# Performance work log

Hardware: AMD Instinct MI355X
Metric: run time of the kernel (lower is better)

Reference implementation:

```python
import jax, jax.numpy as jnp
import numpy as np

Q_HEADS, KV_HEADS, HEAD_SIZE, H, MAX_LEN = 16, 4, 64, 1024, 4096
B, S = 1, 4096


def _rope_tables(max_len, head_size):
    half = head_size // 2
    inv_freq = 1.0 / (10000.0 ** (np.arange(half, dtype=np.float32) / half))
    pos = np.arange(max_len, dtype=np.float32)
    ang = pos[:, None] * inv_freq[None, :]  # [max_len, half]
    return jnp.asarray(np.sin(ang)), jnp.asarray(np.cos(ang))


def setup_inputs() -> dict:
    key = jax.random.key(0)
    ks = jax.random.split(key, 6)
    sc = 1.0 / np.sqrt(H)
    x = jax.random.normal(ks[0], (B, S, H), dtype=jnp.float32)
    wq = jax.random.normal(ks[1], (H, H), dtype=jnp.float32) * sc
    wk = jax.random.normal(ks[2], (H, KV_HEADS * HEAD_SIZE), dtype=jnp.float32) * sc
    wv = jax.random.normal(ks[3], (H, KV_HEADS * HEAD_SIZE), dtype=jnp.float32) * sc
    wo = jax.random.normal(ks[4], (H, H), dtype=jnp.float32) * sc
    sin, cos = _rope_tables(MAX_LEN, HEAD_SIZE)
    full_mask = jnp.tril(jnp.ones((MAX_LEN, MAX_LEN), dtype=bool))
    attention_mask = jnp.ones((B, S), dtype=jnp.int32)
    return {"x": x, "attention_mask": attention_mask, "start": 0,
            "wq": wq, "wk": wk, "wv": wv, "wo": wo,
            "sin": sin, "cos": cos, "full_mask": full_mask}


def _rotate(t, sin, cos, start):
    # t: [b, heads, s, head_size]; interleaved even/odd RoPE
    s = t.shape[2]
    sn = sin[start:start + s, :][None, None, :, :]
    cs = cos[start:start + s, :][None, None, :, :]
    even, odd = t[..., 0::2], t[..., 1::2]
    out_even = cs * even - sn * odd
    out_odd = sn * even + cs * odd
    return jnp.stack((out_even, out_odd), axis=-1).reshape(t.shape)


def _expand_kv(t, group):
    # [b, kv_heads, s, d] -> [b, kv_heads*group, s, d]
    b, kvh, s, d = t.shape
    return jnp.broadcast_to(t[:, :, None], (b, kvh, group, s, d)).reshape(b, kvh * group, s, d)


def reference(x, attention_mask, start, wq, wk, wv, wo, sin, cos, full_mask):
    b, s, _ = x.shape
    group = Q_HEADS // KV_HEADS
    Q = (x @ wq).reshape(b, s, Q_HEADS, HEAD_SIZE).transpose(0, 2, 1, 3)
    K = (x @ wk).reshape(b, s, KV_HEADS, HEAD_SIZE).transpose(0, 2, 1, 3)
    V = (x @ wv).reshape(b, s, KV_HEADS, HEAD_SIZE).transpose(0, 2, 1, 3)
    Q = _rotate(Q, sin, cos, start)
    K = _rotate(K, sin, cos, start)
    K = _expand_kv(K, group)
    V = _expand_kv(V, group)
    z = jnp.einsum('bhqd,bhkd->bhqk', Q, K) / (HEAD_SIZE ** 0.5)
    kv_len = start + s
    mask = full_mask[:s, :kv_len][None, None, :, :]
    amask = (attention_mask[:, :kv_len] != 0)[:, None, None, :]
    mask = mask & amask
    z = jnp.where(mask, z, -1000000.0)
    A = jax.nn.softmax(z, axis=-1)
    ctx = jnp.einsum('bhqk,bhkd->bhqd', A, V)
    q_mask = attention_mask[:, :s].astype(ctx.dtype)[:, None, :, None]
    ctx = ctx * q_mask
    ctx = ctx.transpose(0, 2, 1, 3).reshape(b, s, H)
    return ctx @ wo
```

## Files before the change

kernel.cpp:

```cpp
#include <hip/hip_runtime.h>

typedef __bf16 bf16x8 __attribute__((ext_vector_type(8)));
typedef float f32x4 __attribute__((ext_vector_type(4)));
typedef unsigned int u32x4 __attribute__((ext_vector_type(4)));

typedef const void __attribute__((address_space(1)))* gas1;
typedef void __attribute__((address_space(3)))* las3;

__device__ __forceinline__ unsigned short f2bf(float f) {
  unsigned int u = __builtin_bit_cast(unsigned int, f);
  u += 0x7fffu + ((u >> 16) & 1u);
  return (unsigned short)(u >> 16);
}
__device__ __forceinline__ float bf2f(unsigned short h) {
  unsigned int u = ((unsigned int)h) << 16;
  return __builtin_bit_cast(float, u);
}
__device__ __forceinline__ unsigned int pack2bf(float lo, float hi) {
  return (unsigned int)f2bf(lo) | ((unsigned int)f2bf(hi) << 16);
}
__device__ __forceinline__ unsigned int packtr(float lo, float hi) {
  return __builtin_amdgcn_perm(__builtin_bit_cast(unsigned int, hi),
                               __builtin_bit_cast(unsigned int, lo), 0x07060302u);
}

__global__ __launch_bounds__(256) void prep(const float* __restrict__ x,
                                            const float* __restrict__ wq,
                                            const float* __restrict__ wk,
                                            const float* __restrict__ wv,
                                            const float* __restrict__ wo,
                                            unsigned short* __restrict__ xb,
                                            unsigned short* __restrict__ wtqkv,
                                            unsigned short* __restrict__ wot) {
  __shared__ float tile[32][33];
  const int b = blockIdx.x;
  const int tid = threadIdx.x;
  if (b < 4096) {
    int i = b * 256 + tid;
    float4 v = ((const float4*)x)[i];
    uint2 o;
    o.x = pack2bf(v.x, v.y);
    o.y = pack2bf(v.z, v.w);
    ((uint2*)xb)[i] = o;
    return;
  }
  const float* src;
  unsigned short* dst;
  int R, C, t;
  if (b < 5120)      { t = b - 4096; src = wq; dst = wtqkv;               R = 1024; C = 1024; }
  else if (b < 5376) { t = b - 5120; src = wk; dst = wtqkv + 1024 * 1024; R = 1024; C = 256; }
  else if (b < 5632) { t = b - 5376; src = wv; dst = wtqkv + 1280 * 1024; R = 1024; C = 256; }
  else               { t = b - 5632; src = wo; dst = wot;                 R = 1024; C = 1024; }
  const int ntc = C >> 5;
  const int c0 = (t % ntc) * 32, r0 = (t / ntc) * 32;
  const int tx = tid & 31, ty = tid >> 5;
#pragma unroll
  for (int i = 0; i < 4; ++i)
    tile[ty + i * 8][tx] = src[(r0 + ty + i * 8) * C + c0 + tx];
  __syncthreads();
#pragma unroll
  for (int i = 0; i < 4; ++i)
    dst[(c0 + ty + i * 8) * R + r0 + tx] = f2bf(tile[tx][ty + i * 8]);
}

__global__ __launch_bounds__(256, 2) void gemm_bt2(const unsigned short* __restrict__ A,
                                                   const unsigned short* __restrict__ Bt,
                                                   void* __restrict__ Cout,
                                                   int M, int N, int K, int outF32) {
  __shared__ __align__(16) unsigned short Als[128 * 32];
  __shared__ __align__(16) unsigned short Bls[128 * 32];
  const int tid = threadIdx.x;
  const int wave = tid >> 6, lane = tid & 63;
  const int lgrp = lane >> 4, lmod = lane & 15;
  const int wm = (wave & 1) * 64, wn = (wave >> 1) * 64;
  const int m0 = blockIdx.y * 128, n0 = blockIdx.x * 128;

  f32x4 acc[4][4] = {};

  for (int k0 = 0; k0 < K; k0 += 32) {
    __syncthreads();
#pragma unroll
    for (int it = 0; it < 2; ++it) {
      int idx = tid + it * 256;
      int rr = idx >> 2, cc = (idx & 3) * 8;
      __builtin_amdgcn_global_load_lds((gas1)(const void*)&A[(size_t)(m0 + rr) * K + k0 + cc],
                                       (las3)(void*)&Als[(it * 256 + wave * 64) * 8], 16, 0, 0);
      __builtin_amdgcn_global_load_lds((gas1)(const void*)&Bt[(size_t)(n0 + rr) * K + k0 + cc],
                                       (las3)(void*)&Bls[(it * 256 + wave * 64) * 8], 16, 0, 0);
    }
    __syncthreads();
    bf16x8 af[4], bfr[4];
#pragma unroll
    for (int mi = 0; mi < 4; ++mi)
      af[mi] = __builtin_bit_cast(bf16x8, *(const u32x4*)&Als[(wm + mi * 16 + lmod) * 32 + lgrp * 8]);
#pragma unroll
    for (int ni = 0; ni < 4; ++ni)
      bfr[ni] = __builtin_bit_cast(bf16x8, *(const u32x4*)&Bls[(wn + ni * 16 + lmod) * 32 + lgrp * 8]);
#pragma unroll
    for (int mi = 0; mi < 4; ++mi)
#pragma unroll
      for (int ni = 0; ni < 4; ++ni)
        acc[mi][ni] = __builtin_amdgcn_mfma_f32_16x16x32_bf16(af[mi], bfr[ni], acc[mi][ni], 0, 0, 0);
  }

#pragma unroll
  for (int mi = 0; mi < 4; ++mi)
#pragma unroll
    for (int ni = 0; ni < 4; ++ni)
#pragma unroll
      for (int r = 0; r < 4; ++r) {
        int row = m0 + wm + mi * 16 + lgrp * 4 + r;
        int col = n0 + wn + ni * 16 + lmod;
        float v = acc[mi][ni][r];
        if (outF32) ((float*)Cout)[(size_t)row * N + col] = v;
        else ((unsigned short*)Cout)[(size_t)row * N + col] = f2bf(v);
      }
}

__global__ __launch_bounds__(256) void rope_vt(const unsigned short* __restrict__ qkv,
                                               const float* __restrict__ sinT,
                                               const float* __restrict__ cosT,
                                               unsigned short* __restrict__ Qh,
                                               unsigned short* __restrict__ Kh,
                                               unsigned short* __restrict__ Vt) {
  __shared__ unsigned short tile[32][33];
  const int b = blockIdx.x;
  const int tid = threadIdx.x;
  if (b < 5120) {
    const float qscale = 0.18033688011112042f;
    int u = b * 256 + tid;
    int s = u / 320, cu = u % 320;
    int col = cu * 4;
    uint2 pr = *(const uint2*)&qkv[s * 1536 + col];
    float e0 = bf2f((unsigned short)(pr.x & 0xffff));
    float o0 = bf2f((unsigned short)(pr.x >> 16));
    float e1 = bf2f((unsigned short)(pr.y & 0xffff));
    float o1 = bf2f((unsigned short)(pr.y >> 16));
    if (col < 1024) {
      int h = col >> 6, d = col & 63, i0 = d >> 1;
      float sn0 = sinT[s * 32 + i0], cs0 = cosT[s * 32 + i0];
      float sn1 = sinT[s * 32 + i0 + 1], cs1 = cosT[s * 32 + i0 + 1];
      uint2 w;
      w.x = pack2bf((cs0 * e0 - sn0 * o0) * qscale, (sn0 * e0 + cs0 * o0) * qscale);
      w.y = pack2bf((cs1 * e1 - sn1 * o1) * qscale, (sn1 * e1 + cs1 * o1) * qscale);
      *(uint2*)&Qh[(h * 4096 + s) * 64 + d] = w;
    } else {
      int c = col - 1024;
      int h = c >> 6, d = c & 63, i0 = d >> 1;
      float sn0 = sinT[s * 32 + i0], cs0 = cosT[s * 32 + i0];
      float sn1 = sinT[s * 32 + i0 + 1], cs1 = cosT[s * 32 + i0 + 1];
      uint2 w;
      w.x = pack2bf(cs0 * e0 - sn0 * o0, sn0 * e0 + cs0 * o0);
      w.y = pack2bf(cs1 * e1 - sn1 * o1, sn1 * e1 + cs1 * o1);
      *(uint2*)&Kh[(h * 4096 + s) * 64 + d] = w;
    }
    return;
  }
  int t = b - 5120;
  int h = t >> 8, rem = t & 255;
  int d0 = (rem >> 7) * 32, s0 = (rem & 127) * 32;
  int tx = tid & 31, ty = tid >> 5;
#pragma unroll
  for (int i = 0; i < 4; ++i)
    tile[ty + i * 8][tx] = qkv[(s0 + ty + i * 8) * 1536 + 1280 + h * 64 + d0 + tx];
  __syncthreads();
#pragma unroll
  for (int i = 0; i < 4; ++i)
    Vt[(h * 64 + d0 + ty + i * 8) * 4096 + s0 + tx] = tile[tx][ty + i * 8];
}

__global__ __launch_bounds__(256, 2) void attn3(const unsigned short* __restrict__ Qh,
                                                const unsigned short* __restrict__ Kh,
                                                const unsigned short* __restrict__ Vt,
                                                unsigned short* __restrict__ ctx) {
  __shared__ __align__(16) unsigned short Kls[128 * 68];
  __shared__ __align__(16) unsigned short Vls[64 * 136];
  const int bx = blockIdx.x;
  const int head = bx & 15;
  const int qidx = bx >> 4;
  const int qb = (qidx < 16) ? (31 - qidx) : (qidx - 16);
  const int kvh = head >> 2;
  const int tid = threadIdx.x;
  const int wave = tid >> 6, lane = tid & 63;
  const int lgrp = lane >> 4, lmod = lane & 15;
  const int qbase = qb * 128;

  const unsigned short* Kg = Kh + (size_t)kvh * 4096 * 64;
  const unsigned short* Vg = Vt + (size_t)kvh * 64 * 4096;

  bf16x8 qf[2][2];
  int qrow[2];
#pragma unroll
  for (int qt = 0; qt < 2; ++qt) {
    qrow[qt] = qbase + wave * 32 + qt * 16 + lmod;
    const unsigned short* Qg = Qh + ((size_t)head * 4096 + qrow[qt]) * 64;
    qf[qt][0] = __builtin_bit_cast(bf16x8, *(const u32x4*)&Qg[lgrp * 8]);
    qf[qt][1] = __builtin_bit_cast(bf16x8, *(const u32x4*)&Qg[32 + lgrp * 8]);
  }

  const int kbase = (8 * (lmod >> 2) + (lmod & 3)) * 68 + lgrp * 8;
  const int vbase = lmod * 136 + lgrp * 8;

  f32x4 accO[2][4] = {};
  float m_i[2] = {-3e38f, -3e38f}, l_i[2] = {0.f, 0.f};

  for (int kc = 0; kc <= qb; ++kc) {
    const int kb = kc * 128;
    __syncthreads();
#pragma unroll
    for (int i = 0; i < 4; ++i) {
      int ii = tid + i * 256;
      int r = ii >> 3, sg = (ii & 7) * 8;
      u32x4 dK = *(const u32x4*)&Kg[(size_t)(kb + r) * 64 + sg];
      uint2* pd = (uint2*)&Kls[r * 68 + sg];
      pd[0] = make_uint2(dK[0], dK[1]);
      pd[1] = make_uint2(dK[2], dK[3]);
    }
#pragma unroll
    for (int i = 0; i < 4; ++i) {
      int ii = tid + i * 256;
      int r = ii >> 4, sg = (ii & 15) * 8;
      *(u32x4*)&Vls[r * 136 + sg] = *(const u32x4*)&Vg[(size_t)r * 4096 + kb + sg];
    }
    __syncthreads();

    f32x4 s[4][2][2];
#pragma unroll
    for (int g = 0; g < 4; ++g)
#pragma unroll
      for (int t = 0; t < 2; ++t) {
        const unsigned short* ka = &Kls[kbase + (32 * g + 4 * t) * 68];
        uint2 a0 = *(const uint2*)&ka[0];
        uint2 a1 = *(const uint2*)&ka[4];
        uint2 b0 = *(const uint2*)&ka[32];
        uint2 b1 = *(const uint2*)&ka[36];
        u32x4 lo = {a0.x, a0.y, a1.x, a1.y};
        u32x4 hi = {b0.x, b0.y, b1.x, b1.y};
        bf16x8 alo = __builtin_bit_cast(bf16x8, lo);
        bf16x8 ahi = __builtin_bit_cast(bf16x8, hi);
#pragma unroll
        for (int qt = 0; qt < 2; ++qt) {
          f32x4 z = {};
          z = __builtin_amdgcn_mfma_f32_16x16x32_bf16(alo, qf[qt][0], z, 0, 0, 0);
          z = __builtin_amdgcn_mfma_f32_16x16x32_bf16(ahi, qf[qt][1], z, 0, 0, 0);
          s[g][t][qt] = z;
        }
      }

#pragma unroll
    for (int qt = 0; qt < 2; ++qt) {
      if (kb + 127 > qbase + wave * 32 + qt * 16) {
#pragma unroll
        for (int g = 0; g < 4; ++g)
#pragma unroll
          for (int t = 0; t < 2; ++t)
#pragma unroll
            for (int r = 0; r < 4; ++r) {
              int key = kb + 32 * g + 8 * lgrp + 4 * t + r;
              if (key > qrow[qt]) s[g][t][qt][r] = -3e38f;
            }
      }
    }

#pragma unroll
    for (int qt = 0; qt < 2; ++qt) {
      f32x4 v0 = s[0][0][qt], v1 = s[0][1][qt];
#pragma unroll
      for (int g = 1; g < 4; ++g)
#pragma unroll
        for (int r = 0; r < 4; ++r) {
          v0[r] = fmaxf(v0[r], s[g][0][qt][r]);
          v1[r] = fmaxf(v1[r], s[g][1][qt][r]);
        }
      float mx = fmaxf(fmaxf(fmaxf(v0[0], v0[1]), fmaxf(v0[2], v0[3])),
                       fmaxf(fmaxf(v1[0], v1[1]), fmaxf(v1[2], v1[3])));
      mx = fmaxf(mx, __shfl_xor(mx, 16, 64));
      mx = fmaxf(mx, __shfl_xor(mx, 32, 64));
      float mnew = fmaxf(m_i[qt], mx);
      float alpha = __builtin_amdgcn_exp2f(m_i[qt] - mnew);
      m_i[qt] = mnew;
      f32x4 su = {};
#pragma unroll
      for (int g = 0; g < 4; ++g)
#pragma unroll
        for (int t = 0; t < 2; ++t)
#pragma unroll
          for (int r = 0; r < 4; ++r) {
            float ev = __builtin_amdgcn_exp2f(s[g][t][qt][r] - mnew);
            s[g][t][qt][r] = ev;
            su[r] += ev;
          }
      float rs = (su[0] + su[1]) + (su[2] + su[3]);
      rs += __shfl_xor(rs, 16, 64);
      rs += __shfl_xor(rs, 32, 64);
      l_i[qt] = l_i[qt] * alpha + rs;
#pragma unroll
      for (int dt = 0; dt < 4; ++dt)
#pragma unroll
        for (int r = 0; r < 4; ++r) accO[qt][dt][r] *= alpha;
    }

#pragma unroll
    for (int g = 0; g < 4; ++g) {
      bf16x8 pf[2];
#pragma unroll
      for (int qt = 0; qt < 2; ++qt) {
        u32x4 pk;
        pk[0] = packtr(s[g][0][qt][0], s[g][0][qt][1]);
        pk[1] = packtr(s[g][0][qt][2], s[g][0][qt][3]);
        pk[2] = packtr(s[g][1][qt][0], s[g][1][qt][1]);
        pk[3] = packtr(s[g][1][qt][2], s[g][1][qt][3]);
        pf[qt] = __builtin_bit_cast(bf16x8, pk);
      }
#pragma unroll
      for (int dt = 0; dt < 4; ++dt) {
        bf16x8 vf = __builtin_bit_cast(bf16x8, *(const u32x4*)&Vls[vbase + dt * 2176 + 32 * g]);
        accO[0][dt] = __builtin_amdgcn_mfma_f32_16x16x32_bf16(vf, pf[0], accO[0][dt], 0, 0, 0);
        accO[1][dt] = __builtin_amdgcn_mfma_f32_16x16x32_bf16(vf, pf[1], accO[1][dt], 0, 0, 0);
      }
    }
  }

#pragma unroll
  for (int qt = 0; qt < 2; ++qt) {
    float inv = 1.f / l_i[qt];
#pragma unroll
    for (int dt = 0; dt < 4; ++dt) {
      uint2 o;
      o.x = pack2bf(accO[qt][dt][0] * inv, accO[qt][dt][1] * inv);
      o.y = pack2bf(accO[qt][dt][2] * inv, accO[qt][dt][3] * inv);
      *(uint2*)&ctx[(size_t)qrow[qt] * 1024 + head * 64 + dt * 16 + lgrp * 4] = o;
    }
  }
}

extern "C" void kernel_launch(void* const* d_in, const int* in_sizes, int n_in,
                              void* d_out, int out_size, void* d_ws, size_t ws_size,
                              hipStream_t stream) {
  const float* x    = (const float*)d_in[0];
  const float* wq   = (const float*)d_in[3];
  const float* wk   = (const float*)d_in[4];
  const float* wv   = (const float*)d_in[5];
  const float* wo   = (const float*)d_in[6];
  const float* sinT = (const float*)d_in[7];
  const float* cosT = (const float*)d_in[8];

  unsigned short* ws    = (unsigned short*)d_ws;
  unsigned short* xb    = ws;
  unsigned short* wtqkv = xb + 4096 * 1024;
  unsigned short* wot   = wtqkv + 1536 * 1024;
  unsigned short* qkv   = wot + 1024 * 1024;
  unsigned short* Qh    = qkv + 4096 * 1536;
  unsigned short* Kh    = Qh + 16 * 4096 * 64;
  unsigned short* Vt    = Kh + 4 * 4096 * 64;
  unsigned short* ctx   = Vt + 4 * 64 * 4096;
  float* out = (float*)d_out;

  prep<<<6656, 256, 0, stream>>>(x, wq, wk, wv, wo, xb, wtqkv, wot);
  gemm_bt2<<<dim3(12, 32), 256, 0, stream>>>(xb, wtqkv, qkv, 4096, 1536, 1024, 0);
  rope_vt<<<6144, 256, 0, stream>>>(qkv, sinT, cosT, Qh, Kh, Vt);
  attn3<<<dim3(512), 256, 0, stream>>>(Qh, Kh, Vt, ctx);
  gemm_bt2<<<dim3(8, 32), 256, 0, stream>>>(ctx, wot, out, 4096, 1024, 1024, 1);
}
```

Baseline: 258.1 us.

## Fuse RoPE and V transpose into QKV GEMM epilogue; retile GEMMs and attention

The QKV projection GEMM now writes rotated, scaled Q and K and transposed V directly, which removes the separate rope_vt kernel and the intermediate qkv buffer round trip. sin and cos are interleaved into one float2 table during prep. Both GEMMs move to 128x64 tiles with more blocks and higher occupancy bounds. Attention switches to 128-thread blocks covering 64 query rows each, with a new causal ordering of query blocks for load balance. The epilogue stores are scattered 2-byte writes and use shuffles, and the smaller tiles reduce data reuse per block.

```diff
diff --git a/kernel.cpp b/kernel.cpp
--- a/kernel.cpp
+++ b/kernel.cpp
@@ -29,9 +29,12 @@
                                             const float* __restrict__ wk,
                                             const float* __restrict__ wv,
                                             const float* __restrict__ wo,
+                                            const float* __restrict__ sinT,
+                                            const float* __restrict__ cosT,
                                             unsigned short* __restrict__ xb,
                                             unsigned short* __restrict__ wtqkv,
-                                            unsigned short* __restrict__ wot) {
+                                            unsigned short* __restrict__ wot,
+                                            float2* __restrict__ scT) {
   __shared__ float tile[32][33];
   const int b = blockIdx.x;
   const int tid = threadIdx.x;
@@ -44,6 +47,11 @@
     ((uint2*)xb)[i] = o;
     return;
   }
+  if (b >= 6656) {
+    int idx = (b - 6656) * 256 + tid;
+    scT[idx] = make_float2(sinT[idx], cosT[idx]);
+    return;
+  }
   const float* src;
   unsigned short* dst;
   int R, C, t;
@@ -63,113 +71,144 @@
     dst[(c0 + ty + i * 8) * R + r0 + tx] = f2bf(tile[tx][ty + i * 8]);
 }
 
-__global__ __launch_bounds__(256, 2) void gemm_bt2(const unsigned short* __restrict__ A,
+__global__ __launch_bounds__(256, 3) void gemm_qkv(const unsigned short* __restrict__ A,
                                                    const unsigned short* __restrict__ Bt,
-                                                   void* __restrict__ Cout,
-                                                   int M, int N, int K, int outF32) {
+                                                   const float2* __restrict__ scT,
+                                                   unsigned short* __restrict__ Qh,
+                                                   unsigned short* __restrict__ Kh,
+                                                   unsigned short* __restrict__ Vt) {
   __shared__ __align__(16) unsigned short Als[128 * 32];
-  __shared__ __align__(16) unsigned short Bls[128 * 32];
+  __shared__ __align__(16) unsigned short Bls[64 * 32];
+  const int K = 1024;
   const int tid = threadIdx.x;
   const int wave = tid >> 6, lane = tid & 63;
   const int lgrp = lane >> 4, lmod = lane & 15;
-  const int wm = (wave & 1) * 64, wn = (wave >> 1) * 64;
-  const int m0 = blockIdx.y * 128, n0 = blockIdx.x * 128;
-
-  f32x4 acc[4][4] = {};
+  const int wm = (wave & 1) * 64, wn = (wave >> 1) * 32;
+  const int m0 = blockIdx.y * 128, n0 = blockIdx.x * 64;
+  const int rr = tid >> 2, cc = (tid & 3) * 8;
+
+  f32x4 acc[4][2] = {};
 
   for (int k0 = 0; k0 < K; k0 += 32) {
     __syncthreads();
 #pragma unroll
     for (int it = 0; it < 2; ++it) {
       int idx = tid + it * 256;
-      int rr = idx >> 2, cc = (idx & 3) * 8;
-      __builtin_amdgcn_global_load_lds((gas1)(const void*)&A[(size_t)(m0 + rr) * K + k0 + cc],
+      __builtin_amdgcn_global_load_lds((gas1)(const void*)&A[(size_t)(m0 + (idx >> 2)) * K + k0 + cc],
                                        (las3)(void*)&Als[(it * 256 + wave * 64) * 8], 16, 0, 0);
-      __builtin_amdgcn_global_load_lds((gas1)(const void*)&Bt[(size_t)(n0 + rr) * K + k0 + cc],
-                                       (las3)(void*)&Bls[(it * 256 + wave * 64) * 8], 16, 0, 0);
-    }
-    __syncthreads();
-    bf16x8 af[4], bfr[4];
+    }
+    __builtin_amdgcn_global_load_lds((gas1)(const void*)&Bt[(size_t)(n0 + rr) * K + k0 + cc],
+                                     (las3)(void*)&Bls[(wave * 64) * 8], 16, 0, 0);
+    __syncthreads();
+    bf16x8 af[4], bfr[2];
 #pragma unroll
     for (int mi = 0; mi < 4; ++mi)
       af[mi] = __builtin_bit_cast(bf16x8, *(const u32x4*)&Als[(wm + mi * 16 + lmod) * 32 + lgrp * 8]);
 #pragma unroll
-    for (int ni = 0; ni < 4; ++ni)
+    for (int ni = 0; ni < 2; ++ni)
       bfr[ni] = __builtin_bit_cast(bf16x8, *(const u32x4*)&Bls[(wn + ni * 16 + lmod) * 32 + lgrp * 8]);
 #pragma unroll
     for (int mi = 0; mi < 4; ++mi)
 #pragma unroll
-      for (int ni = 0; ni < 4; ++ni)
+      for (int ni = 0; ni < 2; ++ni)
         acc[mi][ni] = __builtin_amdgcn_mfma_f32_16x16x32_bf16(af[mi], bfr[ni], acc[mi][ni], 0, 0, 0);
   }
 
+  const int cbase = n0;
+  if (cbase >= 1280) {
+    const int kvh = (cbase - 1280) >> 6;
+#pragma unroll
+    for (int mi = 0; mi < 4; ++mi)
+#pragma unroll
+      for (int ni = 0; ni < 2; ++ni) {
+        int d = wn + ni * 16 + lmod;
+        int s = m0 + wm + mi * 16 + lgrp * 4;
+        uint2 o;
+        o.x = pack2bf(acc[mi][ni][0], acc[mi][ni][1]);
+        o.y = pack2bf(acc[mi][ni][2], acc[mi][ni][3]);
+        *(uint2*)&Vt[((size_t)(kvh * 64 + d)) * 4096 + s] = o;
+      }
+    return;
+  }
+
+  const float qscale = 0.18033688011112042f;
+  const bool isQ = (cbase < 1024);
+  const int h = isQ ? (cbase >> 6) : ((cbase - 1024) >> 6);
+  unsigned short* dstbase = isQ ? Qh : Kh;
+  const bool evn = (lmod & 1) == 0;
 #pragma unroll
   for (int mi = 0; mi < 4; ++mi)
 #pragma unroll
-    for (int ni = 0; ni < 4; ++ni)
+    for (int ni = 0; ni < 2; ++ni) {
+      int d = ((cbase & 63) + wn + ni * 16 + lmod) & 63;
+      int i = d >> 1;
+#pragma unroll
+      for (int r = 0; r < 4; ++r) {
+        float v = acc[mi][ni][r];
+        float pp = __shfl_xor(v, 1, 64);
+        int rl = wm + mi * 16 + lgrp * 4 + r;
+        float2 sc = scT[(size_t)(m0 + rl) * 32 + i];
+        float e = evn ? v : pp, o = evn ? pp : v;
+        float outv = evn ? (sc.y * e - sc.x * o) : (sc.x * e + sc.y * o);
+        if (isQ) outv *= qscale;
+        dstbase[((size_t)h * 4096 + m0 + rl) * 64 + d] = f2bf(outv);
+      }
+    }
+}
+
+__global__ __launch_bounds__(256, 3) void gemm_out(const unsigned short* __restrict__ A,
+                                                   const unsigned short* __restrict__ Bt,
+                                                   float* __restrict__ Cout) {
+  __shared__ __align__(16) unsigned short Als[128 * 32];
+  __shared__ __align__(16) unsigned short Bls[64 * 32];
+  const int K = 1024, N = 1024;
+  const int tid = threadIdx.x;
+  const int wave = tid >> 6, lane = tid & 63;
+  const int lgrp = lane >> 4, lmod = lane & 15;
+  const int wm = (wave & 1) * 64, wn = (wave >> 1) * 32;
+  const int m0 = blockIdx.y * 128, n0 = blockIdx.x * 64;
+  const int rr = tid >> 2, cc = (tid & 3) * 8;
+
+  f32x4 acc[4][2] = {};
+
+  for (int k0 = 0; k0 < K; k0 += 32) {
+    __syncthreads();
+#pragma unroll
+    for (int it = 0; it < 2; ++it) {
+      int idx = tid + it * 256;
+      __builtin_amdgcn_global_load_lds((gas1)(const void*)&A[(size_t)(m0 + (idx >> 2)) * K + k0 + cc],
+                                       (las3)(void*)&Als[(it * 256 + wave * 64) * 8], 16, 0, 0);
+    }
+    __builtin_amdgcn_global_load_lds((gas1)(const void*)&Bt[(size_t)(n0 + rr) * K + k0 + cc],
+                                     (las3)(void*)&Bls[(wave * 64) * 8], 16, 0, 0);
+    __syncthreads();
+    bf16x8 af[4], bfr[2];
+#pragma unroll
+    for (int mi = 0; mi < 4; ++mi)
+      af[mi] = __builtin_bit_cast(bf16x8, *(const u32x4*)&Als[(wm + mi * 16 + lmod) * 32 + lgrp * 8]);
+#pragma unroll
+    for (int ni = 0; ni < 2; ++ni)
+      bfr[ni] = __builtin_bit_cast(bf16x8, *(const u32x4*)&Bls[(wn + ni * 16 + lmod) * 32 + lgrp * 8]);
+#pragma unroll
+    for (int mi = 0; mi < 4; ++mi)
+#pragma unroll
+      for (int ni = 0; ni < 2; ++ni)
+        acc[mi][ni] = __builtin_amdgcn_mfma_f32_16x16x32_bf16(af[mi], bfr[ni], acc[mi][ni], 0, 0, 0);
+  }
+
+#pragma unroll
+  for (int mi = 0; mi < 4; ++mi)
+#pragma unroll
+    for (int ni = 0; ni < 2; ++ni)
 #pragma unroll
       for (int r = 0; r < 4; ++r) {
         int row = m0 + wm + mi * 16 + lgrp * 4 + r;
         int col = n0 + wn + ni * 16 + lmod;
-        float v = acc[mi][ni][r];
-        if (outF32) ((float*)Cout)[(size_t)row * N + col] = v;
-        else ((unsigned short*)Cout)[(size_t)row * N + col] = f2bf(v);
-      }
-}
-
-__global__ __launch_bounds__(256) void rope_vt(const unsigned short* __restrict__ qkv,
-                                               const float* __restrict__ sinT,
-                                               const float* __restrict__ cosT,
-                                               unsigned short* __restrict__ Qh,
-                                               unsigned short* __restrict__ Kh,
-                                               unsigned short* __restrict__ Vt) {
-  __shared__ unsigned short tile[32][33];
-  const int b = blockIdx.x;
-  const int tid = threadIdx.x;
-  if (b < 5120) {
-    const float qscale = 0.18033688011112042f;
-    int u = b * 256 + tid;
-    int s = u / 320, cu = u % 320;
-    int col = cu * 4;
-    uint2 pr = *(const uint2*)&qkv[s * 1536 + col];
-    float e0 = bf2f((unsigned short)(pr.x & 0xffff));
-    float o0 = bf2f((unsigned short)(pr.x >> 16));
-    float e1 = bf2f((unsigned short)(pr.y & 0xffff));
-    float o1 = bf2f((unsigned short)(pr.y >> 16));
-    if (col < 1024) {
-      int h = col >> 6, d = col & 63, i0 = d >> 1;
-      float sn0 = sinT[s * 32 + i0], cs0 = cosT[s * 32 + i0];
-      float sn1 = sinT[s * 32 + i0 + 1], cs1 = cosT[s * 32 + i0 + 1];
-      uint2 w;
-      w.x = pack2bf((cs0 * e0 - sn0 * o0) * qscale, (sn0 * e0 + cs0 * o0) * qscale);
-      w.y = pack2bf((cs1 * e1 - sn1 * o1) * qscale, (sn1 * e1 + cs1 * o1) * qscale);
-      *(uint2*)&Qh[(h * 4096 + s) * 64 + d] = w;
-    } else {
-      int c = col - 1024;
-      int h = c >> 6, d = c & 63, i0 = d >> 1;
-      float sn0 = sinT[s * 32 + i0], cs0 = cosT[s * 32 + i0];
-      float sn1 = sinT[s * 32 + i0 + 1], cs1 = cosT[s * 32 + i0 + 1];
-      uint2 w;
-      w.x = pack2bf(cs0 * e0 - sn0 * o0, sn0 * e0 + cs0 * o0);
-      w.y = pack2bf(cs1 * e1 - sn1 * o1, sn1 * e1 + cs1 * o1);
-      *(uint2*)&Kh[(h * 4096 + s) * 64 + d] = w;
-    }
-    return;
-  }
-  int t = b - 5120;
-  int h = t >> 8, rem = t & 255;
-  int d0 = (rem >> 7) * 32, s0 = (rem & 127) * 32;
-  int tx = tid & 31, ty = tid >> 5;
-#pragma unroll
-  for (int i = 0; i < 4; ++i)
-    tile[ty + i * 8][tx] = qkv[(s0 + ty + i * 8) * 1536 + 1280 + h * 64 + d0 + tx];
-  __syncthreads();
-#pragma unroll
-  for (int i = 0; i < 4; ++i)
-    Vt[(h * 64 + d0 + ty + i * 8) * 4096 + s0 + tx] = tile[tx][ty + i * 8];
-}
-
-__global__ __launch_bounds__(256, 2) void attn3(const unsigned short* __restrict__ Qh,
+        Cout[(size_t)row * N + col] = acc[mi][ni][r];
+      }
+}
+
+__global__ __launch_bounds__(128, 4) void attn7(const unsigned short* __restrict__ Qh,
                                                 const unsigned short* __restrict__ Kh,
                                                 const unsigned short* __restrict__ Vt,
                                                 unsigned short* __restrict__ ctx) {
@@ -178,12 +217,17 @@
   const int bx = blockIdx.x;
   const int head = bx & 15;
   const int qidx = bx >> 4;
-  const int qb = (qidx < 16) ? (31 - qidx) : (qidx - 16);
+  int qb64;
+  if (qidx < 16)      qb64 = 63 - qidx;
+  else if (qidx < 32) qb64 = 16 + qidx - 16 + 16;
+  else if (qidx < 48) qb64 = 63 - qidx;
+  else                qb64 = qidx - 48;
   const int kvh = head >> 2;
   const int tid = threadIdx.x;
   const int wave = tid >> 6, lane = tid & 63;
   const int lgrp = lane >> 4, lmod = lane & 15;
-  const int qbase = qb * 128;
+  const int qbase = qb64 * 64;
+  const int nch = (qb64 >> 1) + 1;
 
   const unsigned short* Kg = Kh + (size_t)kvh * 4096 * 64;
   const unsigned short* Vg = Vt + (size_t)kvh * 64 * 4096;
@@ -204,12 +248,12 @@
   f32x4 accO[2][4] = {};
   float m_i[2] = {-3e38f, -3e38f}, l_i[2] = {0.f, 0.f};
 
-  for (int kc = 0; kc <= qb; ++kc) {
+  for (int kc = 0; kc < nch; ++kc) {
     const int kb = kc * 128;
     __syncthreads();
 #pragma unroll
-    for (int i = 0; i < 4; ++i) {
-      int ii = tid + i * 256;
+    for (int i = 0; i < 8; ++i) {
+      int ii = tid + i * 128;
       int r = ii >> 3, sg = (ii & 7) * 8;
       u32x4 dK = *(const u32x4*)&Kg[(size_t)(kb + r) * 64 + sg];
       uint2* pd = (uint2*)&Kls[r * 68 + sg];
@@ -217,8 +261,8 @@
       pd[1] = make_uint2(dK[2], dK[3]);
     }
 #pragma unroll
-    for (int i = 0; i < 4; ++i) {
-      int ii = tid + i * 256;
+    for (int i = 0; i < 8; ++i) {
+      int ii = tid + i * 128;
       int r = ii >> 4, sg = (ii & 15) * 8;
       *(u32x4*)&Vls[r * 136 + sg] = *(const u32x4*)&Vg[(size_t)r * 4096 + kb + sg];
     }
@@ -349,16 +393,15 @@
   unsigned short* xb    = ws;
   unsigned short* wtqkv = xb + 4096 * 1024;
   unsigned short* wot   = wtqkv + 1536 * 1024;
-  unsigned short* qkv   = wot + 1024 * 1024;
-  unsigned short* Qh    = qkv + 4096 * 1536;
+  unsigned short* Qh    = wot + 1024 * 1024;
   unsigned short* Kh    = Qh + 16 * 4096 * 64;
   unsigned short* Vt    = Kh + 4 * 4096 * 64;
   unsigned short* ctx   = Vt + 4 * 64 * 4096;
+  float2* scT           = (float2*)(ctx + 4096 * 1024);
   float* out = (float*)d_out;
 
-  prep<<<6656, 256, 0, stream>>>(x, wq, wk, wv, wo, xb, wtqkv, wot);
-  gemm_bt2<<<dim3(12, 32), 256, 0, stream>>>(xb, wtqkv, qkv, 4096, 1536, 1024, 0);
-  rope_vt<<<6144, 256, 0, stream>>>(qkv, sinT, cosT, Qh, Kh, Vt);
-  attn3<<<dim3(512), 256, 0, stream>>>(Qh, Kh, Vt, ctx);
-  gemm_bt2<<<dim3(8, 32), 256, 0, stream>>>(ctx, wot, out, 4096, 1024, 1024, 1);
-}
+  prep<<<7168, 256, 0, stream>>>(x, wq, wk, wv, wo, sinT, cosT, xb, wtqkv, wot, scT);
+  gemm_qkv<<<dim3(24, 32), 256, 0, stream>>>(xb, wtqkv, scT, Qh, Kh, Vt);
+  attn7<<<dim3(1024), 128, 0, stream>>>(Qh, Kh, Vt, ctx);
+  gemm_out<<<dim3(16, 32), 256, 0, stream>>>(ctx, wot, out);
+}
```

After: 269.1 us. 1.04x slower.
